# Kernel tuning notes

Measured on AMD Instinct MI355X. Metric: run time of the kernel, lower is better.

Reference implementation:

```python
import jax, jax.numpy as jnp
import numpy as np

B, N, K, H = 2, 2048, 48, 128
NIN = 2 * H          # num_in = 2*num_hidden (ProteinMPNN wiring)
FF = 4 * H           # PositionWiseFeedForward hidden
SCALE = 30.0
EPS = 1e-5           # torch LayerNorm default eps


def _ln(x, g, b):
    m = jnp.mean(x, axis=-1, keepdims=True)
    v = jnp.mean((x - m) ** 2, axis=-1, keepdims=True)
    return (x - m) / jnp.sqrt(v + EPS) * g + b


def _gelu(x):
    return jax.nn.gelu(x, approximate=False)  # torch.nn.GELU default (erf)


def _lin(x, W, b):
    return x @ W + b


def setup_inputs() -> dict:
    key = jax.random.key(0)
    ks = jax.random.split(key, 24)
    s = 0.05
    inp = {
        "h_V": jax.random.normal(ks[0], (B, N, H), jnp.float32),
        "h_E": jax.random.normal(ks[1], (B, N, K, H), jnp.float32),
        "E_idx": jax.random.randint(ks[2], (B, N, K), 0, N, jnp.int64),
        "mask_V": jnp.ones((B, N), jnp.float32),
        "mask_attend": jnp.ones((B, N, K), jnp.float32),
        # message MLP (node update): W1 in = H + NIN = 3H
        "W1": jax.random.normal(ks[3], (3 * H, H), jnp.float32) * s,
        "b1": jnp.zeros((H,), jnp.float32),
        "W2": jax.random.normal(ks[4], (H, H), jnp.float32) * s,
        "b2": jnp.zeros((H,), jnp.float32),
        "W3": jax.random.normal(ks[5], (H, H), jnp.float32) * s,
        "b3": jnp.zeros((H,), jnp.float32),
        # PositionWiseFeedForward
        "Wd_in": jax.random.normal(ks[6], (H, FF), jnp.float32) * s,
        "bd_in": jnp.zeros((FF,), jnp.float32),
        "Wd_out": jax.random.normal(ks[7], (FF, H), jnp.float32) * s,
        "bd_out": jnp.zeros((H,), jnp.float32),
        # edge-update MLP: W11 in = H + NIN = 3H
        "W11": jax.random.normal(ks[8], (3 * H, H), jnp.float32) * s,
        "b11": jnp.zeros((H,), jnp.float32),
        "W12": jax.random.normal(ks[9], (H, H), jnp.float32) * s,
        "b12": jnp.zeros((H,), jnp.float32),
        "W13": jax.random.normal(ks[10], (H, H), jnp.float32) * s,
        "b13": jnp.zeros((H,), jnp.float32),
        # LayerNorms
        "n1g": jnp.ones((H,), jnp.float32), "n1b": jnp.zeros((H,), jnp.float32),
        "n2g": jnp.ones((H,), jnp.float32), "n2b": jnp.zeros((H,), jnp.float32),
        "n3g": jnp.ones((H,), jnp.float32), "n3b": jnp.zeros((H,), jnp.float32),
    }
    return inp


def reference(h_V, h_E, E_idx, mask_V, mask_attend,
              W1, b1, W2, b2, W3, b3,
              Wd_in, bd_in, Wd_out, bd_out,
              W11, b11, W12, b12, W13, b13,
              n1g, n1b, n2g, n2b, n3g, n3b):
    gather = jax.vmap(lambda hv, idx: hv[idx])  # [B,N,H],[B,N,K] -> [B,N,K,H]

    # --- node update: cat_neighbors_nodes + expand + 3-layer GELU MLP ---
    h_nb = gather(h_V, E_idx)                                   # [B,N,K,H]
    hV_exp = jnp.broadcast_to(h_V[:, :, None, :], h_nb.shape)   # [B,N,K,H]
    h_EV = jnp.concatenate([hV_exp, h_E, h_nb], axis=-1)        # [B,N,K,3H]
    h_msg = _lin(_gelu(_lin(_gelu(_lin(h_EV, W1, b1)), W2, b2)), W3, b3)
    h_msg = mask_attend[..., None] * h_msg
    dh = jnp.sum(h_msg, axis=-2) / SCALE                        # masked-sum reduce
    h_V = _ln(h_V + dh, n1g, n1b)

    # --- position-wise FFN ---
    dh = _lin(_gelu(_lin(h_V, Wd_in, bd_in)), Wd_out, bd_out)
    h_V = _ln(h_V + dh, n2g, n2b)
    h_V = mask_V[..., None] * h_V

    # --- edge update (not last layer) ---
    h_nb2 = gather(h_V, E_idx)
    hV_exp2 = jnp.broadcast_to(h_V[:, :, None, :], h_nb2.shape)
    h_EV2 = jnp.concatenate([hV_exp2, h_E, h_nb2], axis=-1)     # [B,N,K,3H]
    h_msg2 = _lin(_gelu(_lin(_gelu(_lin(h_EV2, W11, b11)), W12, b12)), W13, b13)
    h_E = _ln(h_E + h_msg2, n3g, n3b)
    return (h_V, h_E)
```

## Files before the change

kernel.cpp:

```cpp
#include <hip/hip_runtime.h>
#include <hip/hip_bf16.h>
#include <stdint.h>

#define XP2 264
#define MP 136
#define EPIP 132
#define FFP 520

typedef __attribute__((ext_vector_type(8))) short bf16x8;
typedef __attribute__((ext_vector_type(4))) float f32x4;

__device__ __forceinline__ f32x4 mfma16(bf16x8 a, bf16x8 b, f32x4 c) {
  return __builtin_amdgcn_mfma_f32_16x16x32_bf16(a, b, c, 0, 0, 0);
}

__device__ __forceinline__ uint16_t f2b(float f) {
  union { __hip_bfloat16 h; uint16_t u; } v;
  v.h = __float2bfloat16(f);
  return v.u;
}
__device__ __forceinline__ uint32_t pk2f(float a, float b) {
  union { __hip_bfloat162 h; uint32_t u; } v;
  v.h = __float22bfloat162_rn(make_float2(a, b));
  return v.u;
}
__device__ __forceinline__ float gelu_f(float x) {
  float u = __builtin_fmaf(x * x, 0.044715f, 1.0f);
  float e = __builtin_amdgcn_exp2f(-2.302585093f * x * u);
  return x * __builtin_amdgcn_rcpf(1.0f + e);
}

__global__ __launch_bounds__(256) void k_prep(
    const float* __restrict__ hV,
    const float* __restrict__ W1, const float* __restrict__ W2, const float* __restrict__ W3,
    const float* __restrict__ WdIn, const float* __restrict__ WdOut,
    const float* __restrict__ W11, const float* __restrict__ W12, const float* __restrict__ W13,
    uint16_t* __restrict__ hVb,
    uint16_t* __restrict__ W1t, uint16_t* __restrict__ W2t, uint16_t* __restrict__ W3t,
    uint16_t* __restrict__ WdInT, uint16_t* __restrict__ WdOutT,
    uint16_t* __restrict__ W11t, uint16_t* __restrict__ W12t, uint16_t* __restrict__ W13t) {
  int i = blockIdx.x * 256 + threadIdx.x;
  if (i < 524288) { hVb[i] = f2b(hV[i]); return; }
  int j = i - 524288;
  if (j < 49152) { int n = j / 384, k = j - n * 384; W1t[j] = f2b(W1[k * 128 + n]); return; }
  j -= 49152;
  if (j < 16384) { int n = j >> 7, k = j & 127; W2t[j] = f2b(W2[k * 128 + n]); return; }
  j -= 16384;
  if (j < 16384) { int n = j >> 7, k = j & 127; W3t[j] = f2b(W3[k * 128 + n]); return; }
  j -= 16384;
  if (j < 65536) { int n = j >> 7, k = j & 127; WdInT[j] = f2b(WdIn[k * 512 + n]); return; }
  j -= 65536;
  if (j < 65536) { int n = j >> 9, k = j & 511; WdOutT[j] = f2b(WdOut[k * 128 + n]); return; }
  j -= 65536;
  if (j < 49152) { int n = j / 384, k = j - n * 384; W11t[j] = f2b(W11[k * 128 + n]); return; }
  j -= 49152;
  if (j < 16384) { int n = j >> 7, k = j & 127; W12t[j] = f2b(W12[k * 128 + n]); return; }
  j -= 16384;
  if (j < 16384) { int n = j >> 7, k = j & 127; W13t[j] = f2b(W13[k * 128 + n]); return; }
}

__global__ __launch_bounds__(256) void k_vec(
    const uint16_t* __restrict__ Xb, const uint16_t* __restrict__ Wt,
    float* __restrict__ C) {
  const int tid = threadIdx.x;
  const int lane = tid & 63, w = tid >> 6, l15 = lane & 15, lg = lane >> 4;
  const int row0 = blockIdx.x * 64 + w * 16;
  f32x4 acc[8] = {};
#pragma unroll
  for (int ks = 0; ks < 4; ++ks) {
    bf16x8 a = *(const bf16x8*)(Xb + (row0 + l15) * 128 + ks * 32 + lg * 8);
#pragma unroll
    for (int j = 0; j < 8; ++j) {
      bf16x8 bb = *(const bf16x8*)(Wt + (j * 16 + l15) * 384 + ks * 32 + lg * 8);
      acc[j] = mfma16(a, bb, acc[j]);
    }
  }
#pragma unroll
  for (int j = 0; j < 8; ++j)
#pragma unroll
    for (int r = 0; r < 4; ++r)
      C[(row0 + lg * 4 + r) * 128 + j * 16 + l15] = acc[j][r];
}

#define BUILD_XT(GSRC)                                                              \
  do {                                                                              \
    for (int idx = tid; idx < 48 * 32; idx += 256) {                                \
      int k_ = idx >> 5;                                                            \
      int c_ = idx & 31;                                                            \
      uint4 v_;                                                                     \
      if (c_ < 16) {                                                                \
        const float* s_ = hE + (size_t)(bn * 48 + k_) * 128 + (c_ << 3);            \
        float4 f0_ = *(const float4*)s_;                                            \
        float4 f1_ = *(const float4*)(s_ + 4);                                      \
        v_ = make_uint4(pk2f(f0_.x, f0_.y), pk2f(f0_.z, f0_.w),                     \
                        pk2f(f1_.x, f1_.y), pk2f(f1_.z, f1_.w));                    \
      } else {                                                                      \
        v_ = *(const uint4*)((GSRC) + (size_t)nbr[k_] * 128 + ((c_ - 16) << 3));    \
      }                                                                             \
      *(uint4*)(xt + k_ * XP2 + (c_ << 3)) = v_;                                    \
    }                                                                               \
  } while (0)

#define LAYER256(WT, ACC)                                                           \
  do {                                                                              \
    const uint16_t* wr0_ = (WT) + (w * 32 + l15) * 384 + 128 + lg * 8;              \
    const uint16_t* wr1_ = wr0_ + 16 * 384;                                         \
    _Pragma("unroll 2") for (int ks = 0; ks < 8; ++ks) {                            \
      bf16x8 bA_ = *(const bf16x8*)(wr0_ + ks * 32);                                \
      bf16x8 bB_ = *(const bf16x8*)(wr1_ + ks * 32);                                \
      _Pragma("unroll") for (int m = 0; m < 3; ++m) {                               \
        bf16x8 a_ = *(const bf16x8*)(xt + (m * 16 + l15) * XP2 + ks * 32 + lg * 8); \
        ACC[m][0] = mfma16(a_, bA_, ACC[m][0]);                                     \
        ACC[m][1] = mfma16(a_, bB_, ACC[m][1]);                                     \
      }                                                                             \
    }                                                                               \
  } while (0)

#define LAYER128(WT, ASRC, ACC)                                                     \
  do {                                                                              \
    const uint16_t* wr0_ = (WT) + (w * 32 + l15) * 128 + lg * 8;                    \
    const uint16_t* wr1_ = wr0_ + 16 * 128;                                         \
    _Pragma("unroll") for (int ks = 0; ks < 4; ++ks) {                              \
      bf16x8 bA_ = *(const bf16x8*)(wr0_ + ks * 32);                                \
      bf16x8 bB_ = *(const bf16x8*)(wr1_ + ks * 32);                                \
      _Pragma("unroll") for (int m = 0; m < 3; ++m) {                               \
        bf16x8 a_ = *(const bf16x8*)((ASRC) + (m * 16 + l15) * MP + ks * 32 + lg * 8); \
        ACC[m][0] = mfma16(a_, bA_, ACC[m][0]);                                     \
        ACC[m][1] = mfma16(a_, bB_, ACC[m][1]);                                     \
      }                                                                              \
    }                                                                               \
  } while (0)

#define GSTORE(ACC, BIAS, DST)                                                      \
  do {                                                                              \
    float bA_ = (BIAS)[w * 32 + l15];                                               \
    float bB_ = (BIAS)[w * 32 + 16 + l15];                                          \
    _Pragma("unroll") for (int m = 0; m < 3; ++m)                                   \
    _Pragma("unroll") for (int r = 0; r < 4; ++r) {                                 \
      int row_ = m * 16 + lg * 4 + r;                                               \
      (DST)[row_ * MP + w * 32 + l15] = f2b(gelu_f(ACC[m][0][r] + bA_));            \
      (DST)[row_ * MP + w * 32 + 16 + l15] = f2b(gelu_f(ACC[m][1][r] + bB_));       \
    }                                                                               \
  } while (0)

#define ACC_INIT(ACC, CV)                                                           \
  do {                                                                              \
    float c0_ = (CV)[bn * 128 + w * 32 + l15];                                      \
    float c1_ = (CV)[bn * 128 + w * 32 + 16 + l15];                                 \
    _Pragma("unroll") for (int m = 0; m < 3; ++m) {                                 \
      ACC[m][0] = (f32x4){c0_, c0_, c0_, c0_};                                      \
      ACC[m][1] = (f32x4){c1_, c1_, c1_, c1_};                                      \
    }                                                                               \
  } while (0)

__global__ __launch_bounds__(256, 6) void k_node(
    const float* __restrict__ hV, const float* __restrict__ hE,
    const int* __restrict__ eidx, const float* __restrict__ maskA,
    const float* __restrict__ bias1, const float* __restrict__ bias2,
    const float* __restrict__ bias3,
    const float* __restrict__ g1, const float* __restrict__ be1,
    const uint16_t* __restrict__ hVb, const float* __restrict__ C1,
    const uint16_t* __restrict__ W1t, const uint16_t* __restrict__ W2t,
    const uint16_t* __restrict__ W3t,
    float* __restrict__ hV1, uint16_t* __restrict__ hV1b) {
  __shared__ __align__(16) unsigned char lds[26880];
  uint16_t* xt = (uint16_t*)lds;
  uint16_t* midA = (uint16_t*)lds;
  uint16_t* midB = (uint16_t*)(lds + 13056);
  int* nbr = (int*)(lds + 26112);
  float* dh = (float*)(lds + 26368);

  const int tid = threadIdx.x;
  const int lane = tid & 63;
  const int w = tid >> 6;
  const int l15 = lane & 15;
  const int lg = lane >> 4;
  const int bn = blockIdx.x;
  const int b = bn >> 11;

  if (tid < 48) nbr[tid] = (b << 11) + eidx[bn * 48 + tid];
  __syncthreads();

  BUILD_XT(hVb);
  __syncthreads();

  f32x4 acc1[3][2];
  ACC_INIT(acc1, C1);
  LAYER256(W1t, acc1);
  __syncthreads();
  GSTORE(acc1, bias1, midA);
  __syncthreads();

  f32x4 acc2[3][2] = {};
  LAYER128(W2t, midA, acc2);
  GSTORE(acc2, bias2, midB);
  __syncthreads();

  f32x4 acc3[3][2] = {};
  LAYER128(W3t, midB, acc3);

  {
    float bA = bias3[w * 32 + l15];
    float bB = bias3[w * 32 + 16 + l15];
    float s0 = 0.f, s1 = 0.f;
#pragma unroll
    for (int m = 0; m < 3; ++m)
#pragma unroll
      for (int r = 0; r < 4; ++r) {
        int row = m * 16 + lg * 4 + r;
        float mk = maskA[bn * 48 + row];
        s0 += (acc3[m][0][r] + bA) * mk;
        s1 += (acc3[m][1][r] + bB) * mk;
      }
    s0 += __shfl_xor(s0, 16); s0 += __shfl_xor(s0, 32);
    s1 += __shfl_xor(s1, 16); s1 += __shfl_xor(s1, 32);
    if (lg == 0) { dh[w * 32 + l15] = s0; dh[w * 32 + 16 + l15] = s1; }
  }
  __syncthreads();

  if (w == 0) {
    const float inv = 1.0f / 30.0f;
    float x0 = hV[bn * 128 + lane] + dh[lane] * inv;
    float x1 = hV[bn * 128 + 64 + lane] + dh[64 + lane] * inv;
    float s = x0 + x1, q = x0 * x0 + x1 * x1;
#pragma unroll
    for (int off = 1; off < 64; off <<= 1) {
      s += __shfl_xor(s, off);
      q += __shfl_xor(q, off);
    }
    float mean = s * (1.0f / 128.0f);
    float var = q * (1.0f / 128.0f) - mean * mean;
    float rstd = rsqrtf(var + 1e-5f);
    float y0 = (x0 - mean) * rstd * g1[lane] + be1[lane];
    float y1 = (x1 - mean) * rstd * g1[64 + lane] + be1[64 + lane];
    hV1[bn * 128 + lane] = y0;
    hV1[bn * 128 + 64 + lane] = y1;
    hV1b[bn * 128 + lane] = f2b(y0);
    hV1b[bn * 128 + 64 + lane] = f2b(y1);
  }
}

__global__ __launch_bounds__(256, 2) void k_ffn(
    const float* __restrict__ hV1, const uint16_t* __restrict__ hV1b,
    const float* __restrict__ maskV,
    const float* __restrict__ bdin, const float* __restrict__ bdout,
    const float* __restrict__ g2, const float* __restrict__ be2,
    const uint16_t* __restrict__ WdInT, const uint16_t* __restrict__ WdOutT,
    float* __restrict__ outV, uint16_t* __restrict__ hV2b) {
  __shared__ __align__(16) unsigned char lds[20992];
  uint16_t* xa = (uint16_t*)lds;
  uint16_t* mf = (uint16_t*)(lds + 4352);
  float* epi = (float*)(lds + 4352);

  const int tid = threadIdx.x;
  const int lane = tid & 63;
  const int w = tid >> 6;
  const int l15 = lane & 15;
  const int lg = lane >> 4;
  const int node0 = blockIdx.x * 16;

  {
    int row = tid >> 4, c = tid & 15;
    *(uint4*)(xa + row * 136 + (c << 3)) =
        *(const uint4*)(hV1b + (node0 + row) * 128 + (c << 3));
  }
  __syncthreads();

  f32x4 acc[8] = {};
  {
    const uint16_t* ar = xa + l15 * 136 + lg * 8;
#pragma unroll
    for (int ks = 0; ks < 4; ++ks) {
      bf16x8 a = *(const bf16x8*)(ar + ks * 32);
#pragma unroll
      for (int j = 0; j < 8; ++j) {
        bf16x8 bb = *(const bf16x8*)(WdInT + ((w * 8 + j) * 16 + l15) * 128 + ks * 32 + lg * 8);
        acc[j] = mfma16(a, bb, acc[j]);
      }
    }
  }
#pragma unroll
  for (int j = 0; j < 8; ++j) {
    int col = (w * 8 + j) * 16 + l15;
    float bs = bdin[col];
#pragma unroll
    for (int r = 0; r < 4; ++r) {
      int row = lg * 4 + r;
      mf[row * FFP + col] = f2b(gelu_f(acc[j][r] + bs));
    }
  }
  __syncthreads();

  f32x4 acc2[2] = {};
  {
    const uint16_t* mr = mf + l15 * FFP + lg * 8;
#pragma unroll 4
    for (int ks = 0; ks < 16; ++ks) {
      bf16x8 a = *(const bf16x8*)(mr + ks * 32);
#pragma unroll
      for (int t = 0; t < 2; ++t) {
        bf16x8 bb = *(const bf16x8*)(WdOutT + ((w * 2 + t) * 16 + l15) * 512 + ks * 32 + lg * 8);
        acc2[t] = mfma16(a, bb, acc2[t]);
      }
    }
  }
  __syncthreads();
#pragma unroll
  for (int t = 0; t < 2; ++t) {
    int col = (w * 2 + t) * 16 + l15;
    float bs = bdout[col];
#pragma unroll
    for (int r = 0; r < 4; ++r) {
      int row = lg * 4 + r;
      epi[row * EPIP + col] = acc2[t][r] + bs;
    }
  }
  __syncthreads();

#pragma unroll
  for (int rr = 0; rr < 4; ++rr) {
    int row = w * 4 + rr;
    int node = node0 + row;
    float x0 = epi[row * EPIP + lane] + hV1[node * 128 + lane];
    float x1 = epi[row * EPIP + 64 + lane] + hV1[node * 128 + 64 + lane];
    float s = x0 + x1, q = x0 * x0 + x1 * x1;
#pragma unroll
    for (int off = 1; off < 64; off <<= 1) {
      s += __shfl_xor(s, off);
      q += __shfl_xor(q, off);
    }
    float mean = s * (1.0f / 128.0f);
    float var = q * (1.0f / 128.0f) - mean * mean;
    float rstd = rsqrtf(var + 1e-5f);
    float mv = maskV[node];
    float y0 = mv * ((x0 - mean) * rstd * g2[lane] + be2[lane]);
    float y1 = mv * ((x1 - mean) * rstd * g2[64 + lane] + be2[64 + lane]);
    outV[node * 128 + lane] = y0;
    outV[node * 128 + 64 + lane] = y1;
    hV2b[node * 128 + lane] = f2b(y0);
    hV2b[node * 128 + 64 + lane] = f2b(y1);
  }
}

__global__ __launch_bounds__(256, 6) void k_edge(
    const float* __restrict__ hE, const int* __restrict__ eidx,
    const float* __restrict__ bias1, const float* __restrict__ bias2,
    const float* __restrict__ bias3,
    const float* __restrict__ g3, const float* __restrict__ be3,
    const uint16_t* __restrict__ hV2b, const float* __restrict__ C2,
    const uint16_t* __restrict__ W1t, const uint16_t* __restrict__ W2t,
    const uint16_t* __restrict__ W3t,
    float* __restrict__ outE) {
  __shared__ __align__(16) unsigned char lds[26304];
  uint16_t* xt = (uint16_t*)lds;
  uint16_t* midA = (uint16_t*)lds;
  uint16_t* midB = (uint16_t*)(lds + 13056);
  int* nbr = (int*)(lds + 26112);
  float* part_s = (float*)lds;
  float* part_q = (float*)(lds + 768);
  float* mstd = (float*)(lds + 1536);

  const int tid = threadIdx.x;
  const int lane = tid & 63;
  const int w = tid >> 6;
  const int l15 = lane & 15;
  const int lg = lane >> 4;
  const int bn = blockIdx.x;
  const int b = bn >> 11;

  if (tid < 48) nbr[tid] = (b << 11) + eidx[bn * 48 + tid];
  __syncthreads();

  BUILD_XT(hV2b);
  __syncthreads();

  f32x4 acc1[3][2];
  ACC_INIT(acc1, C2);
  LAYER256(W1t, acc1);
  __syncthreads();
  GSTORE(acc1, bias1, midA);
  __syncthreads();

  f32x4 acc2[3][2] = {};
  LAYER128(W2t, midA, acc2);
  GSTORE(acc2, bias2, midB);
  __syncthreads();

  f32x4 acc3[3][2] = {};
  LAYER128(W3t, midB, acc3);

  const float bA = bias3[w * 32 + l15];
  const float bB = bias3[w * 32 + 16 + l15];

  float xs0[3][4], xs1[3][4];
#pragma unroll
  for (int m = 0; m < 3; ++m)
#pragma unroll
    for (int r = 0; r < 4; ++r) {
      int row = m * 16 + lg * 4 + r;
      size_t e = (size_t)bn * 48 + row;
      xs0[m][r] = acc3[m][0][r] + bA + hE[e * 128 + w * 32 + l15];
      xs1[m][r] = acc3[m][1][r] + bB + hE[e * 128 + w * 32 + 16 + l15];
      float s = xs0[m][r] + xs1[m][r];
      float q = xs0[m][r] * xs0[m][r] + xs1[m][r] * xs1[m][r];
      s += __shfl_xor(s, 1); q += __shfl_xor(q, 1);
      s += __shfl_xor(s, 2); q += __shfl_xor(q, 2);
      s += __shfl_xor(s, 4); q += __shfl_xor(q, 4);
      s += __shfl_xor(s, 8); q += __shfl_xor(q, 8);
      if (l15 == 0) { part_s[row * 4 + w] = s; part_q[row * 4 + w] = q; }
    }
  __syncthreads();

  if (tid < 48) {
    float s = part_s[tid * 4] + part_s[tid * 4 + 1] + part_s[tid * 4 + 2] + part_s[tid * 4 + 3];
    float q = part_q[tid * 4] + part_q[tid * 4 + 1] + part_q[tid * 4 + 2] + part_q[tid * 4 + 3];
    float mean = s * (1.0f / 128.0f);
    float var = q * (1.0f / 128.0f) - mean * mean;
    mstd[tid * 2] = mean;
    mstd[tid * 2 + 1] = rsqrtf(var + 1e-5f);
  }
  __syncthreads();

  const float gA = g3[w * 32 + l15], beA = be3[w * 32 + l15];
  const float gB = g3[w * 32 + 16 + l15], beB = be3[w * 32 + 16 + l15];
#pragma unroll
  for (int m = 0; m < 3; ++m)
#pragma unroll
    for (int r = 0; r < 4; ++r) {
      int row = m * 16 + lg * 4 + r;
      size_t e = (size_t)bn * 48 + row;
      float mean = mstd[row * 2];
      float rstd = mstd[row * 2 + 1];
      outE[e * 128 + w * 32 + l15] = (xs0[m][r] - mean) * rstd * gA + beA;
      outE[e * 128 + w * 32 + 16 + l15] = (xs1[m][r] - mean) * rstd * gB + beB;
    }
}

extern "C" void kernel_launch(void* const* d_in, const int* in_sizes, int n_in,
                              void* d_out, int out_size, void* d_ws, size_t ws_size,
                              hipStream_t stream) {
  const float* hV = (const float*)d_in[0];
  const float* hE = (const float*)d_in[1];
  const int* eidx = (const int*)d_in[2];
  const float* maskV = (const float*)d_in[3];
  const float* maskA = (const float*)d_in[4];
  const float* W1 = (const float*)d_in[5];   const float* b1 = (const float*)d_in[6];
  const float* W2 = (const float*)d_in[7];   const float* b2 = (const float*)d_in[8];
  const float* W3 = (const float*)d_in[9];   const float* b3 = (const float*)d_in[10];
  const float* WdIn = (const float*)d_in[11];  const float* bdin = (const float*)d_in[12];
  const float* WdOut = (const float*)d_in[13]; const float* bdout = (const float*)d_in[14];
  const float* W11 = (const float*)d_in[15]; const float* b11 = (const float*)d_in[16];
  const float* W12 = (const float*)d_in[17]; const float* b12 = (const float*)d_in[18];
  const float* W13 = (const float*)d_in[19]; const float* b13 = (const float*)d_in[20];
  const float* n1g = (const float*)d_in[21]; const float* n1b = (const float*)d_in[22];
  const float* n2g = (const float*)d_in[23]; const float* n2b = (const float*)d_in[24];
  const float* n3g = (const float*)d_in[25]; const float* n3b = (const float*)d_in[26];

  char* ws = (char*)d_ws;
  uint16_t* hVb    = (uint16_t*)(ws + 0);
  uint16_t* W1t    = (uint16_t*)(ws + 1048576);
  uint16_t* W2t    = (uint16_t*)(ws + 1146880);
  uint16_t* W3t    = (uint16_t*)(ws + 1179648);
  uint16_t* WdInT  = (uint16_t*)(ws + 1212416);
  uint16_t* WdOutT = (uint16_t*)(ws + 1343488);
  uint16_t* W11t   = (uint16_t*)(ws + 1474560);
  uint16_t* W12t   = (uint16_t*)(ws + 1572864);
  uint16_t* W13t   = (uint16_t*)(ws + 1605632);
  float*    hV1    = (float*)(ws + 1638400);
  uint16_t* hV1b   = (uint16_t*)(ws + 3735552);
  uint16_t* hV2b   = (uint16_t*)(ws + 4784128);
  float*    C1     = (float*)(ws + 5832704);
  float*    C2     = (float*)(ws + 7929856);

  float* outV = (float*)d_out;
  float* outE = (float*)d_out + 524288;

  k_prep<<<3200, 256, 0, stream>>>(hV, W1, W2, W3, WdIn, WdOut, W11, W12, W13,
                                   hVb, W1t, W2t, W3t, WdInT, WdOutT, W11t, W12t, W13t);
  k_vec<<<64, 256, 0, stream>>>(hVb, W1t, C1);
  k_node<<<4096, 256, 0, stream>>>(hV, hE, eidx, maskA, b1, b2, b3, n1g, n1b,
                                   hVb, C1, W1t, W2t, W3t, hV1, hV1b);
  k_ffn<<<256, 256, 0, stream>>>(hV1, hV1b, maskV, bdin, bdout, n2g, n2b,
                                 WdInT, WdOutT, outV, hV2b);
  k_vec<<<64, 256, 0, stream>>>(hV2b, W11t, C2);
  k_edge<<<4096, 256, 0, stream>>>(hE, eidx, b11, b12, b13, n3g, n3b,
                                   hV2b, C2, W11t, W12t, W13t, outE);
}
```

Baseline: 226.1 us.

## Make node/edge kernels persistent with register-staged double-buffered edge tile prefetch

```diff
diff --git a/kernel.cpp b/kernel.cpp
--- a/kernel.cpp
+++ b/kernel.cpp
@@ -4,8 +4,8 @@
 
 #define XP2 264
 #define MP 136
+#define FFP 520
 #define EPIP 132
-#define FFP 520
 
 typedef __attribute__((ext_vector_type(8))) short bf16x8;
 typedef __attribute__((ext_vector_type(4))) float f32x4;
@@ -61,7 +61,7 @@
 
 __global__ __launch_bounds__(256) void k_vec(
     const uint16_t* __restrict__ Xb, const uint16_t* __restrict__ Wt,
-    float* __restrict__ C) {
+    const float* __restrict__ bias, float* __restrict__ C) {
   const int tid = threadIdx.x;
   const int lane = tid & 63, w = tid >> 6, l15 = lane & 15, lg = lane >> 4;
   const int row0 = blockIdx.x * 64 + w * 16;
@@ -76,32 +76,46 @@
     }
   }
 #pragma unroll
-  for (int j = 0; j < 8; ++j)
+  for (int j = 0; j < 8; ++j) {
+    float bs = bias[j * 16 + l15];
 #pragma unroll
     for (int r = 0; r < 4; ++r)
-      C[(row0 + lg * 4 + r) * 128 + j * 16 + l15] = acc[j][r];
-}
-
-#define BUILD_XT(GSRC)                                                              \
-  do {                                                                              \
-    for (int idx = tid; idx < 48 * 32; idx += 256) {                                \
-      int k_ = idx >> 5;                                                            \
-      int c_ = idx & 31;                                                            \
-      uint4 v_;                                                                     \
-      if (c_ < 16) {                                                                \
-        const float* s_ = hE + (size_t)(bn * 48 + k_) * 128 + (c_ << 3);            \
-        float4 f0_ = *(const float4*)s_;                                            \
-        float4 f1_ = *(const float4*)(s_ + 4);                                      \
-        v_ = make_uint4(pk2f(f0_.x, f0_.y), pk2f(f0_.z, f0_.w),                     \
-                        pk2f(f1_.x, f1_.y), pk2f(f1_.z, f1_.w));                    \
-      } else {                                                                      \
-        v_ = *(const uint4*)((GSRC) + (size_t)nbr[k_] * 128 + ((c_ - 16) << 3));    \
+      C[(row0 + lg * 4 + r) * 128 + j * 16 + l15] = acc[j][r] + bs;
+  }
+}
+
+#define STAGE_LOAD(TB, GSRC)                                                        \
+  do {                                                                              \
+    if (cc < 16) {                                                                  \
+      _Pragma("unroll") for (int it = 0; it < 6; ++it) {                            \
+        const float* s_ = hE + (size_t)((TB) + kr0 + it * 8) * 128 + cc * 8;        \
+        sA[it] = *(const float4*)s_;                                                \
+        sB[it] = *(const float4*)(s_ + 4);                                          \
       }                                                                             \
-      *(uint4*)(xt + k_ * XP2 + (c_ << 3)) = v_;                                    \
-    }                                                                               \
-  } while (0)
-
-#define LAYER256(WT, ACC)                                                           \
+    } else {                                                                        \
+      _Pragma("unroll") for (int it = 0; it < 6; ++it) {                            \
+        int e_ = (TB) + kr0 + it * 8;                                               \
+        int nb_ = ((e_ >= 98304) ? 2048 : 0) + eidx[e_];                            \
+        *(uint4*)&sA[it] = *(const uint4*)((GSRC) + (size_t)nb_ * 128 + (cc - 16) * 8); \
+      }                                                                             \
+    }                                                                               \
+  } while (0)
+
+#define STAGE_WRITE(BUF)                                                            \
+  do {                                                                              \
+    if (cc < 16) {                                                                  \
+      _Pragma("unroll") for (int it = 0; it < 6; ++it) {                            \
+        uint4 v_ = make_uint4(pk2f(sA[it].x, sA[it].y), pk2f(sA[it].z, sA[it].w),   \
+                              pk2f(sB[it].x, sB[it].y), pk2f(sB[it].z, sB[it].w));  \
+        *(uint4*)((BUF) + (kr0 + it * 8) * XP2 + cc * 8) = v_;                      \
+      }                                                                             \
+    } else {                                                                        \
+      _Pragma("unroll") for (int it = 0; it < 6; ++it)                              \
+        *(uint4*)((BUF) + (kr0 + it * 8) * XP2 + cc * 8) = *(uint4*)&sA[it];        \
+    }                                                                               \
+  } while (0)
+
+#define LAYER256(WT, XSRC, ACC)                                                     \
   do {                                                                              \
     const uint16_t* wr0_ = (WT) + (w * 32 + l15) * 384 + 128 + lg * 8;              \
     const uint16_t* wr1_ = wr0_ + 16 * 384;                                         \
@@ -109,7 +123,7 @@
       bf16x8 bA_ = *(const bf16x8*)(wr0_ + ks * 32);                                \
       bf16x8 bB_ = *(const bf16x8*)(wr1_ + ks * 32);                                \
       _Pragma("unroll") for (int m = 0; m < 3; ++m) {                               \
-        bf16x8 a_ = *(const bf16x8*)(xt + (m * 16 + l15) * XP2 + ks * 32 + lg * 8); \
+        bf16x8 a_ = *(const bf16x8*)((XSRC) + (m * 16 + l15) * XP2 + ks * 32 + lg * 8); \
         ACC[m][0] = mfma16(a_, bA_, ACC[m][0]);                                     \
         ACC[m][1] = mfma16(a_, bB_, ACC[m][1]);                                     \
       }                                                                             \
@@ -143,100 +157,126 @@
     }                                                                               \
   } while (0)
 
-#define ACC_INIT(ACC, CV)                                                           \
-  do {                                                                              \
-    float c0_ = (CV)[bn * 128 + w * 32 + l15];                                      \
-    float c1_ = (CV)[bn * 128 + w * 32 + 16 + l15];                                 \
+#define GSTORE0(ACC, DST)                                                           \
+  do {                                                                              \
+    _Pragma("unroll") for (int m = 0; m < 3; ++m)                                   \
+    _Pragma("unroll") for (int r = 0; r < 4; ++r) {                                 \
+      int row_ = m * 16 + lg * 4 + r;                                               \
+      (DST)[row_ * MP + w * 32 + l15] = f2b(gelu_f(ACC[m][0][r]));                  \
+      (DST)[row_ * MP + w * 32 + 16 + l15] = f2b(gelu_f(ACC[m][1][r]));             \
+    }                                                                               \
+  } while (0)
+
+#define ACC_INIT(ACC, CV, ND)                                                       \
+  do {                                                                              \
+    float c0_ = (CV)[(size_t)(ND) * 128 + w * 32 + l15];                            \
+    float c1_ = (CV)[(size_t)(ND) * 128 + w * 32 + 16 + l15];                       \
     _Pragma("unroll") for (int m = 0; m < 3; ++m) {                                 \
       ACC[m][0] = (f32x4){c0_, c0_, c0_, c0_};                                      \
       ACC[m][1] = (f32x4){c1_, c1_, c1_, c1_};                                      \
     }                                                                               \
   } while (0)
 
-__global__ __launch_bounds__(256, 6) void k_node(
+__global__ __launch_bounds__(256, 2) void k_node(
     const float* __restrict__ hV, const float* __restrict__ hE,
     const int* __restrict__ eidx, const float* __restrict__ maskA,
-    const float* __restrict__ bias1, const float* __restrict__ bias2,
-    const float* __restrict__ bias3,
+    const float* __restrict__ bias2, const float* __restrict__ bias3,
     const float* __restrict__ g1, const float* __restrict__ be1,
     const uint16_t* __restrict__ hVb, const float* __restrict__ C1,
     const uint16_t* __restrict__ W1t, const uint16_t* __restrict__ W2t,
     const uint16_t* __restrict__ W3t,
     float* __restrict__ hV1, uint16_t* __restrict__ hV1b) {
-  __shared__ __align__(16) unsigned char lds[26880];
-  uint16_t* xt = (uint16_t*)lds;
-  uint16_t* midA = (uint16_t*)lds;
-  uint16_t* midB = (uint16_t*)(lds + 13056);
-  int* nbr = (int*)(lds + 26112);
-  float* dh = (float*)(lds + 26368);
+  __shared__ __align__(16) unsigned char lds[76800];
+  uint16_t* xtA = (uint16_t*)lds;
+  uint16_t* xtB = (uint16_t*)(lds + 25344);
+  uint16_t* midA = (uint16_t*)(lds + 50688);
+  uint16_t* midB = (uint16_t*)(lds + 63744);
+  float* dh = (float*)(lds + 50688);
 
   const int tid = threadIdx.x;
   const int lane = tid & 63;
   const int w = tid >> 6;
   const int l15 = lane & 15;
   const int lg = lane >> 4;
-  const int bn = blockIdx.x;
-  const int b = bn >> 11;
-
-  if (tid < 48) nbr[tid] = (b << 11) + eidx[bn * 48 + tid];
-  __syncthreads();
-
-  BUILD_XT(hVb);
-  __syncthreads();
-
-  f32x4 acc1[3][2];
-  ACC_INIT(acc1, C1);
-  LAYER256(W1t, acc1);
-  __syncthreads();
-  GSTORE(acc1, bias1, midA);
-  __syncthreads();
-
-  f32x4 acc2[3][2] = {};
-  LAYER128(W2t, midA, acc2);
-  GSTORE(acc2, bias2, midB);
-  __syncthreads();
-
-  f32x4 acc3[3][2] = {};
-  LAYER128(W3t, midB, acc3);
+  const int kr0 = tid >> 5;
+  const int cc = tid & 31;
+
+  float4 sA[6], sB[6];
+  uint16_t* xc = xtA;
+  uint16_t* xn = xtB;
 
   {
-    float bA = bias3[w * 32 + l15];
-    float bB = bias3[w * 32 + 16 + l15];
-    float s0 = 0.f, s1 = 0.f;
-#pragma unroll
-    for (int m = 0; m < 3; ++m)
-#pragma unroll
-      for (int r = 0; r < 4; ++r) {
-        int row = m * 16 + lg * 4 + r;
-        float mk = maskA[bn * 48 + row];
-        s0 += (acc3[m][0][r] + bA) * mk;
-        s1 += (acc3[m][1][r] + bB) * mk;
+    int tile0 = blockIdx.x;
+    STAGE_LOAD(tile0 * 48, hVb);
+    STAGE_WRITE(xc);
+  }
+
+  for (int t = 0; t < 8; ++t) {
+    const int tile = t * 512 + blockIdx.x;
+    const int nd = tile;
+    const int tbase = tile * 48;
+    __syncthreads();
+
+    if (t < 7) STAGE_LOAD((tile + 512) * 48, hVb);
+
+    f32x4 acc1[3][2];
+    ACC_INIT(acc1, C1, nd);
+    LAYER256(W1t, xc, acc1);
+    __syncthreads();
+    GSTORE0(acc1, midA);
+    __syncthreads();
+
+    f32x4 acc2[3][2] = {};
+    LAYER128(W2t, midA, acc2);
+    GSTORE(acc2, bias2, midB);
+    __syncthreads();
+
+    f32x4 acc3[3][2] = {};
+    LAYER128(W3t, midB, acc3);
+
+    if (t < 7) STAGE_WRITE(xn);
+
+    {
+      float bA = bias3[w * 32 + l15];
+      float bB = bias3[w * 32 + 16 + l15];
+      float s0 = 0.f, s1 = 0.f;
+#pragma unroll
+      for (int m = 0; m < 3; ++m)
+#pragma unroll
+        for (int r = 0; r < 4; ++r) {
+          int row = m * 16 + lg * 4 + r;
+          float mk = maskA[tbase + row];
+          s0 += (acc3[m][0][r] + bA) * mk;
+          s1 += (acc3[m][1][r] + bB) * mk;
+        }
+      s0 += __shfl_xor(s0, 16); s0 += __shfl_xor(s0, 32);
+      s1 += __shfl_xor(s1, 16); s1 += __shfl_xor(s1, 32);
+      if (lg == 0) { dh[w * 32 + l15] = s0; dh[w * 32 + 16 + l15] = s1; }
+    }
+    __syncthreads();
+
+    if (w == 0) {
+      const float inv = 1.0f / 30.0f;
+      float x0 = hV[(size_t)nd * 128 + lane] + dh[lane] * inv;
+      float x1 = hV[(size_t)nd * 128 + 64 + lane] + dh[64 + lane] * inv;
+      float s = x0 + x1, q = x0 * x0 + x1 * x1;
+#pragma unroll
+      for (int off = 1; off < 64; off <<= 1) {
+        s += __shfl_xor(s, off);
+        q += __shfl_xor(q, off);
       }
-    s0 += __shfl_xor(s0, 16); s0 += __shfl_xor(s0, 32);
-    s1 += __shfl_xor(s1, 16); s1 += __shfl_xor(s1, 32);
-    if (lg == 0) { dh[w * 32 + l15] = s0; dh[w * 32 + 16 + l15] = s1; }
-  }
-  __syncthreads();
-
-  if (w == 0) {
-    const float inv = 1.0f / 30.0f;
-    float x0 = hV[bn * 128 + lane] + dh[lane] * inv;
-    float x1 = hV[bn * 128 + 64 + lane] + dh[64 + lane] * inv;
-    float s = x0 + x1, q = x0 * x0 + x1 * x1;
-#pragma unroll
-    for (int off = 1; off < 64; off <<= 1) {
-      s += __shfl_xor(s, off);
-      q += __shfl_xor(q, off);
-    }
-    float mean = s * (1.0f / 128.0f);
-    float var = q * (1.0f / 128.0f) - mean * mean;
-    float rstd = rsqrtf(var + 1e-5f);
-    float y0 = (x0 - mean) * rstd * g1[lane] + be1[lane];
-    float y1 = (x1 - mean) * rstd * g1[64 + lane] + be1[64 + lane];
-    hV1[bn * 128 + lane] = y0;
-    hV1[bn * 128 + 64 + lane] = y1;
-    hV1b[bn * 128 + lane] = f2b(y0);
-    hV1b[bn * 128 + 64 + lane] = f2b(y1);
+      float mean = s * (1.0f / 128.0f);
+      float var = q * (1.0f / 128.0f) - mean * mean;
+      float rstd = rsqrtf(var + 1e-5f);
+      float y0 = (x0 - mean) * rstd * g1[lane] + be1[lane];
+      float y1 = (x1 - mean) * rstd * g1[64 + lane] + be1[64 + lane];
+      hV1[(size_t)nd * 128 + lane] = y0;
+      hV1[(size_t)nd * 128 + 64 + lane] = y1;
+      hV1b[(size_t)nd * 128 + lane] = f2b(y0);
+      hV1b[(size_t)nd * 128 + 64 + lane] = f2b(y1);
+    }
+
+    uint16_t* tmp = xc; xc = xn; xn = tmp;
   }
 }
 
@@ -342,98 +382,114 @@
   }
 }
 
-__global__ __launch_bounds__(256, 6) void k_edge(
+__global__ __launch_bounds__(256, 2) void k_edge(
     const float* __restrict__ hE, const int* __restrict__ eidx,
-    const float* __restrict__ bias1, const float* __restrict__ bias2,
-    const float* __restrict__ bias3,
+    const float* __restrict__ bias2, const float* __restrict__ bias3,
     const float* __restrict__ g3, const float* __restrict__ be3,
     const uint16_t* __restrict__ hV2b, const float* __restrict__ C2,
     const uint16_t* __restrict__ W1t, const uint16_t* __restrict__ W2t,
     const uint16_t* __restrict__ W3t,
     float* __restrict__ outE) {
-  __shared__ __align__(16) unsigned char lds[26304];
-  uint16_t* xt = (uint16_t*)lds;
-  uint16_t* midA = (uint16_t*)lds;
-  uint16_t* midB = (uint16_t*)(lds + 13056);
-  int* nbr = (int*)(lds + 26112);
-  float* part_s = (float*)lds;
-  float* part_q = (float*)(lds + 768);
-  float* mstd = (float*)(lds + 1536);
+  __shared__ __align__(16) unsigned char lds[76800];
+  uint16_t* xtA = (uint16_t*)lds;
+  uint16_t* xtB = (uint16_t*)(lds + 25344);
+  uint16_t* midA = (uint16_t*)(lds + 50688);
+  uint16_t* midB = (uint16_t*)(lds + 63744);
+  float* part_s = (float*)(lds + 50688);
+  float* part_q = (float*)(lds + 51456);
+  float* mstd = (float*)(lds + 52224);
 
   const int tid = threadIdx.x;
   const int lane = tid & 63;
   const int w = tid >> 6;
   const int l15 = lane & 15;
   const int lg = lane >> 4;
-  const int bn = blockIdx.x;
-  const int b = bn >> 11;
-
-  if (tid < 48) nbr[tid] = (b << 11) + eidx[bn * 48 + tid];
-  __syncthreads();
-
-  BUILD_XT(hV2b);
-  __syncthreads();
-
-  f32x4 acc1[3][2];
-  ACC_INIT(acc1, C2);
-  LAYER256(W1t, acc1);
-  __syncthreads();
-  GSTORE(acc1, bias1, midA);
-  __syncthreads();
-
-  f32x4 acc2[3][2] = {};
-  LAYER128(W2t, midA, acc2);
-  GSTORE(acc2, bias2, midB);
-  __syncthreads();
-
-  f32x4 acc3[3][2] = {};
-  LAYER128(W3t, midB, acc3);
-
-  const float bA = bias3[w * 32 + l15];
-  const float bB = bias3[w * 32 + 16 + l15];
-
-  float xs0[3][4], xs1[3][4];
-#pragma unroll
-  for (int m = 0; m < 3; ++m)
-#pragma unroll
-    for (int r = 0; r < 4; ++r) {
-      int row = m * 16 + lg * 4 + r;
-      size_t e = (size_t)bn * 48 + row;
-      xs0[m][r] = acc3[m][0][r] + bA + hE[e * 128 + w * 32 + l15];
-      xs1[m][r] = acc3[m][1][r] + bB + hE[e * 128 + w * 32 + 16 + l15];
-      float s = xs0[m][r] + xs1[m][r];
-      float q = xs0[m][r] * xs0[m][r] + xs1[m][r] * xs1[m][r];
-      s += __shfl_xor(s, 1); q += __shfl_xor(q, 1);
-      s += __shfl_xor(s, 2); q += __shfl_xor(q, 2);
-      s += __shfl_xor(s, 4); q += __shfl_xor(q, 4);
-      s += __shfl_xor(s, 8); q += __shfl_xor(q, 8);
-      if (l15 == 0) { part_s[row * 4 + w] = s; part_q[row * 4 + w] = q; }
-    }
-  __syncthreads();
-
-  if (tid < 48) {
-    float s = part_s[tid * 4] + part_s[tid * 4 + 1] + part_s[tid * 4 + 2] + part_s[tid * 4 + 3];
-    float q = part_q[tid * 4] + part_q[tid * 4 + 1] + part_q[tid * 4 + 2] + part_q[tid * 4 + 3];
-    float mean = s * (1.0f / 128.0f);
-    float var = q * (1.0f / 128.0f) - mean * mean;
-    mstd[tid * 2] = mean;
-    mstd[tid * 2 + 1] = rsqrtf(var + 1e-5f);
-  }
-  __syncthreads();
-
-  const float gA = g3[w * 32 + l15], beA = be3[w * 32 + l15];
-  const float gB = g3[w * 32 + 16 + l15], beB = be3[w * 32 + 16 + l15];
-#pragma unroll
-  for (int m = 0; m < 3; ++m)
-#pragma unroll
-    for (int r = 0; r < 4; ++r) {
-      int row = m * 16 + lg * 4 + r;
-      size_t e = (size_t)bn * 48 + row;
-      float mean = mstd[row * 2];
-      float rstd = mstd[row * 2 + 1];
-      outE[e * 128 + w * 32 + l15] = (xs0[m][r] - mean) * rstd * gA + beA;
-      outE[e * 128 + w * 32 + 16 + l15] = (xs1[m][r] - mean) * rstd * gB + beB;
-    }
+  const int kr0 = tid >> 5;
+  const int cc = tid & 31;
+
+  float4 sA[6], sB[6];
+  uint16_t* xc = xtA;
+  uint16_t* xn = xtB;
+
+  {
+    int tile0 = blockIdx.x;
+    STAGE_LOAD(tile0 * 48, hV2b);
+    STAGE_WRITE(xc);
+  }
+
+  for (int t = 0; t < 8; ++t) {
+    const int tile = t * 512 + blockIdx.x;
+    const int nd = tile;
+    const int tbase = tile * 48;
+    __syncthreads();
+
+    if (t < 7) STAGE_LOAD((tile + 512) * 48, hV2b);
+
+    f32x4 acc1[3][2];
+    ACC_INIT(acc1, C2, nd);
+    LAYER256(W1t, xc, acc1);
+    __syncthreads();
+    GSTORE0(acc1, midA);
+    __syncthreads();
+
+    f32x4 acc2[3][2] = {};
+    LAYER128(W2t, midA, acc2);
+    GSTORE(acc2, bias2, midB);
+    __syncthreads();
+
+    f32x4 acc3[3][2] = {};
+    LAYER128(W3t, midB, acc3);
+
+    if (t < 7) STAGE_WRITE(xn);
+
+    const float bA = bias3[w * 32 + l15];
+    const float bB = bias3[w * 32 + 16 + l15];
+
+    float xs0[3][4], xs1[3][4];
+#pragma unroll
+    for (int m = 0; m < 3; ++m)
+#pragma unroll
+      for (int r = 0; r < 4; ++r) {
+        int row = m * 16 + lg * 4 + r;
+        size_t e = (size_t)tbase + row;
+        xs0[m][r] = acc3[m][0][r] + bA + hE[e * 128 + w * 32 + l15];
+        xs1[m][r] = acc3[m][1][r] + bB + hE[e * 128 + w * 32 + 16 + l15];
+        float s = xs0[m][r] + xs1[m][r];
+        float q = xs0[m][r] * xs0[m][r] + xs1[m][r] * xs1[m][r];
+        s += __shfl_xor(s, 1); q += __shfl_xor(q, 1);
+        s += __shfl_xor(s, 2); q += __shfl_xor(q, 2);
+        s += __shfl_xor(s, 4); q += __shfl_xor(q, 4);
+        s += __shfl_xor(s, 8); q += __shfl_xor(q, 8);
+        if (l15 == 0) { part_s[row * 4 + w] = s; part_q[row * 4 + w] = q; }
+      }
+    __syncthreads();
+
+    if (tid < 48) {
+      float s = part_s[tid * 4] + part_s[tid * 4 + 1] + part_s[tid * 4 + 2] + part_s[tid * 4 + 3];
+      float q = part_q[tid * 4] + part_q[tid * 4 + 1] + part_q[tid * 4 + 2] + part_q[tid * 4 + 3];
+      float mean = s * (1.0f / 128.0f);
+      float var = q * (1.0f / 128.0f) - mean * mean;
+      mstd[tid * 2] = mean;
+      mstd[tid * 2 + 1] = rsqrtf(var + 1e-5f);
+    }
+    __syncthreads();
+
+    const float gA = g3[w * 32 + l15], beA = be3[w * 32 + l15];
+    const float gB = g3[w * 32 + 16 + l15], beB = be3[w * 32 + 16 + l15];
+#pragma unroll
+    for (int m = 0; m < 3; ++m)
+#pragma unroll
+      for (int r = 0; r < 4; ++r) {
+        int row = m * 16 + lg * 4 + r;
+        size_t e = (size_t)tbase + row;
+        float mean = mstd[row * 2];
+        float rstd = mstd[row * 2 + 1];
+        outE[e * 128 + w * 32 + l15] = (xs0[m][r] - mean) * rstd * gA + beA;
+        outE[e * 128 + w * 32 + 16 + l15] = (xs1[m][r] - mean) * rstd * gB + beB;
+      }
+
+    uint16_t* tmp = xc; xc = xn; xn = tmp;
+  }
 }
 
 extern "C" void kernel_launch(void* const* d_in, const int* in_sizes, int n_in,
@@ -477,12 +533,12 @@
 
   k_prep<<<3200, 256, 0, stream>>>(hV, W1, W2, W3, WdIn, WdOut, W11, W12, W13,
                                    hVb, W1t, W2t, W3t, WdInT, WdOutT, W11t, W12t, W13t);
-  k_vec<<<64, 256, 0, stream>>>(hVb, W1t, C1);
-  k_node<<<4096, 256, 0, stream>>>(hV, hE, eidx, maskA, b1, b2, b3, n1g, n1b,
-                                   hVb, C1, W1t, W2t, W3t, hV1, hV1b);
+  k_vec<<<64, 256, 0, stream>>>(hVb, W1t, b1, C1);
+  k_node<<<512, 256, 0, stream>>>(hV, hE, eidx, maskA, b2, b3, n1g, n1b,
+                                  hVb, C1, W1t, W2t, W3t, hV1, hV1b);
   k_ffn<<<256, 256, 0, stream>>>(hV1, hV1b, maskV, bdin, bdout, n2g, n2b,
                                  WdInT, WdOutT, outV, hV2b);
-  k_vec<<<64, 256, 0, stream>>>(hV2b, W11t, C2);
-  k_edge<<<4096, 256, 0, stream>>>(hE, eidx, b11, b12, b13, n3g, n3b,
-                                   hV2b, C2, W11t, W12t, W13t, outE);
-}
+  k_vec<<<64, 256, 0, stream>>>(hV2b, W11t, b11, C2);
+  k_edge<<<512, 256, 0, stream>>>(hE, eidx, b12, b13, n3g, n3b,
+                                  hV2b, C2, W11t, W12t, W13t, outE);
+}
```

After: 234.0 us. +3.5%, slower.
